# Optimization experiments

Measured on AMD Instinct MI355X. Metric: run time of the kernel, lower is better.

## Reference

```python
import jax, jax.numpy as jnp
import numpy as np
import math

D = 1024       # feature_dim
H = 4          # n_heads
HD = D // H
T = 512        # vertice frames
S = 512        # audio frames
V3 = 15069     # vertice_dim (5023*3)
NSUB = 8
PERIOD = 25
MAXLEN = 600
DFF = 2 * D
AUD = 768


def _build_alibi(n_head=H, max_seq=MAXLEN, period=PERIOD):
    def slopes(n):
        def p2(n):
            start = 2 ** (-2 ** (-(math.log2(n) - 3)))
            return [start * start ** i for i in range(n)]
        if math.log2(n).is_integer():
            return p2(n)
        c = 2 ** math.floor(math.log2(n))
        return p2(c) + slopes(2 * c)[0::2][: n - c]
    sl = np.array(slopes(n_head), np.float32)
    bias = (np.arange(0, max_seq, period)[:, None].repeat(period, 1).reshape(-1) // period).astype(np.float32)
    bias = -bias[::-1]
    i = np.arange(max_seq)[:, None]
    j = np.arange(max_seq)[None, :]
    idx = np.clip(max_seq - 1 - i + j, 0, max_seq - 1)
    alibi = np.where(j <= i, bias[idx], 0.0).astype(np.float32)
    causal = np.where(j <= i, 0.0, -np.inf).astype(np.float32)
    return causal[None] + sl[:, None, None] * alibi[None]   # [H, maxlen, maxlen]


def _build_pe(d=D, period=PERIOD, max_seq=MAXLEN):
    pos = np.arange(period, dtype=np.float32)[:, None]
    div = np.exp(np.arange(0, d, 2, dtype=np.float32) * (-math.log(10000.0) / d))
    pe = np.zeros((period, d), np.float32)
    pe[:, 0::2] = np.sin(pos * div)
    pe[:, 1::2] = np.cos(pos * div)
    reps = max_seq // period + 1
    return np.tile(pe, (reps, 1))[None]                     # [1, reps*period, d]

_ALIBI = jnp.asarray(_build_alibi())
_PE = jnp.asarray(_build_pe())


def _ln(x, g, b, eps=1e-5):
    m = jnp.mean(x, -1, keepdims=True)
    v = jnp.mean((x - m) ** 2, -1, keepdims=True)
    return (x - m) * jax.lax.rsqrt(v + eps) * g + b


def _mha(q_in, kv_in, Wqkv, bqkv, Wo, bo, add_mask=None, bool_mask=None):
    # torch nn.MultiheadAttention with in_proj [3D, D]; y = x @ W.T + b
    B, Tq, _ = q_in.shape
    Ts = kv_in.shape[1]
    Wq, Wk, Wv = jnp.split(Wqkv, 3, axis=0)
    bq, bk, bv = jnp.split(bqkv, 3)
    q = (q_in @ Wq.T + bq).reshape(B, Tq, H, HD).transpose(0, 2, 1, 3)
    k = (kv_in @ Wk.T + bk).reshape(B, Ts, H, HD).transpose(0, 2, 1, 3)
    v = (kv_in @ Wv.T + bv).reshape(B, Ts, H, HD).transpose(0, 2, 1, 3)
    scores = jnp.einsum('bhtd,bhsd->bhts', q, k) / math.sqrt(HD)
    if add_mask is not None:
        scores = scores + add_mask[None]            # [1,H,Tq,Ts] float additive (ALiBi+causal)
    if bool_mask is not None:
        scores = jnp.where(bool_mask, -jnp.inf, scores)  # True == masked (torch semantics)
    attn = jax.nn.softmax(scores, axis=-1)
    out = jnp.einsum('bhts,bhsd->bhtd', attn, v).transpose(0, 2, 1, 3).reshape(B, Tq, D)
    return out @ Wo.T + bo


def setup_inputs() -> dict:
    key = jax.random.key(0)
    ks = jax.random.split(key, 32)
    rn = lambda k, shape, s: jax.random.normal(k, shape, jnp.float32) * s
    inp = {
        'audio_feat': rn(ks[0], (1, S, AUD), 1.0),
        'vertice': rn(ks[1], (1, T, V3), 0.1),
        'template': rn(ks[2], (1, V3), 0.1),
        'one_hot': jnp.zeros((1, NSUB), jnp.float32).at[0, 0].set(1.0),
        'W_af': rn(ks[3], (D, AUD), 0.02), 'b_af': jnp.zeros((D,), jnp.float32),
        'W_vm': rn(ks[4], (D, V3), 0.02), 'b_vm': jnp.zeros((D,), jnp.float32),
        'W_obj': rn(ks[5], (D, NSUB), 0.02),
        'Wqkv_sa': rn(ks[6], (3 * D, D), 0.02), 'bqkv_sa': jnp.zeros((3 * D,), jnp.float32),
        'Wo_sa': rn(ks[7], (D, D), 0.02), 'bo_sa': jnp.zeros((D,), jnp.float32),
        'Wqkv_ca': rn(ks[8], (3 * D, D), 0.02), 'bqkv_ca': jnp.zeros((3 * D,), jnp.float32),
        'Wo_ca': rn(ks[9], (D, D), 0.02), 'bo_ca': jnp.zeros((D,), jnp.float32),
        'W1': rn(ks[10], (DFF, D), 0.02), 'b1': jnp.zeros((DFF,), jnp.float32),
        'W2': rn(ks[11], (D, DFF), 0.02), 'b2': jnp.zeros((D,), jnp.float32),
        'g1': jnp.ones((D,), jnp.float32), 'be1': jnp.zeros((D,), jnp.float32),
        'g2': jnp.ones((D,), jnp.float32), 'be2': jnp.zeros((D,), jnp.float32),
        'g3': jnp.ones((D,), jnp.float32), 'be3': jnp.zeros((D,), jnp.float32),
        # vertice_map_r is zero-init in the source; use small random so grads are informative
        'W_vr': rn(ks[12], (V3, D), 0.02), 'b_vr': jnp.zeros((V3,), jnp.float32),
    }
    return inp


def reference(audio_feat, vertice, template, one_hot,
              W_af, b_af, W_vm, b_vm, W_obj,
              Wqkv_sa, bqkv_sa, Wo_sa, bo_sa,
              Wqkv_ca, bqkv_ca, Wo_ca, bo_ca,
              W1, b1, W2, b2, g1, be1, g2, be2, g3, be3,
              W_vr, b_vr):
    tmpl = template[:, None, :]                               # [1,1,V3]
    hidden = audio_feat @ W_af.T + b_af                       # [1,S,D]
    style = (one_hot @ W_obj.T)[:, None, :]                   # [1,1,D]
    # teacher-forcing branch with template
    vin = jnp.concatenate([tmpl, vertice[:, :-1]], axis=1) - tmpl
    vin = vin @ W_vm.T + b_vm + style
    vin = vin + _PE[:, :T, :]                                 # PPE, dropout is identity in eval
    tgt_mask = _ALIBI[:, :T, :T]                              # [H,T,T]
    mem_mask = ~jnp.eye(T, S, dtype=bool)                     # True == masked; only diagonal attended
    x = vin
    x = _ln(x + _mha(x, x, Wqkv_sa, bqkv_sa, Wo_sa, bo_sa, add_mask=tgt_mask), g1, be1)
    x = _ln(x + _mha(x, hidden, Wqkv_ca, bqkv_ca, Wo_ca, bo_ca, bool_mask=mem_mask), g2, be2)
    ff = jax.nn.relu(x @ W1.T + b1) @ W2.T + b2
    x = _ln(x + ff, g3, be3)
    vertice_out = x @ W_vr.T + b_vr + tmpl                    # [1,T,V3]
    return vertice_out
```

## Files before the change

kernel.cpp:

```cpp
#include <hip/hip_runtime.h>
#include <math.h>

typedef __attribute__((ext_vector_type(8))) short short8;
typedef __attribute__((ext_vector_type(4))) float f32x4;
typedef unsigned short ushort_t;

#define KVIN 15360

__device__ __forceinline__ ushort_t f2bf(float f) {
  unsigned u = __float_as_uint(f);
  return (ushort_t)((u + 0x7fffu + ((u >> 16) & 1u)) >> 16);
}
__device__ __forceinline__ float bf2f(ushort_t h) {
  return __uint_as_float(((unsigned)h) << 16);
}

__device__ __forceinline__ float blockReduceSum256(float v, float* red) {
  #pragma unroll
  for (int o = 32; o; o >>= 1) v += __shfl_xor(v, o);
  int wid = threadIdx.x >> 6, lane = threadIdx.x & 63;
  if (lane == 0) red[wid] = v;
  __syncthreads();
  v = red[0] + red[1] + red[2] + red[3];
  __syncthreads();
  return v;
}
__device__ __forceinline__ float blockReduceMax256(float v, float* red) {
  #pragma unroll
  for (int o = 32; o; o >>= 1) v = fmaxf(v, __shfl_xor(v, o));
  int wid = threadIdx.x >> 6, lane = threadIdx.x & 63;
  if (lane == 0) red[wid] = v;
  __syncthreads();
  v = fmaxf(fmaxf(red[0], red[1]), fmaxf(red[2], red[3]));
  __syncthreads();
  return v;
}

template <bool BF16B, int BIASM, bool CAUSAL, int GMODE, int ZDIV>
__global__ __launch_bounds__(256, 2) void glds5(
    const ushort_t* __restrict__ A, const void* __restrict__ Bv,
    const float* __restrict__ bias, const float* __restrict__ biasB,
    float* __restrict__ C,
    int N, int K, int lda, int ldb, int ldc,
    int kChunk, long aZ, long bZ, long cZ)
{
  int z, m0, n0;
  if (GMODE == 2) {
    const int id = blockIdx.x, u = id & 7, v = id >> 3;
    m0 = (v & 3) * 128;
    n0 = (((v >> 2) << 3) + u) * 128;
    z = 0;
    if (n0 >= N) return;
  } else if (GMODE == 1) {
    z = blockIdx.x; m0 = blockIdx.y * 128; n0 = blockIdx.z * 128;
  } else {
    z = blockIdx.z; m0 = blockIdx.y * 128; n0 = blockIdx.x * 128;
  }
  if (CAUSAL && n0 > m0 + 127) return;
  __shared__ ushort_t sA[2][4096], sB[2][4096];
  const int tid = threadIdx.x;
  const int ks = ZDIV ? (z % ZDIV) : z;
  const int zb = ZDIV ? (z / ZDIV) : z;
  const int kBeg = kChunk ? ks * kChunk : 0;
  const int kEnd = kChunk ? kBeg + kChunk : K;
  A += (size_t)zb * aZ;
  const ushort_t* Bh = (const ushort_t*)Bv;
  const float*    Bf = (const float*)Bv;
  if (BF16B) Bh += (size_t)zb * bZ; else Bf += (size_t)zb * bZ;
  C += (size_t)z * cZ;

  const int r0 = ((tid >> 6) << 4) | (tid & 15);
  const int q0 = (tid >> 4) & 3;
  const int r1 = r0 + 64;
  const ushort_t* pA0 = A + (size_t)(m0 + r0) * lda + (q0 << 3);
  const ushort_t* pA1 = A + (size_t)(m0 + r1) * lda + (q0 << 3);
  const int gn0 = n0 + r0, gn1 = n0 + r1;
  const bool bok0 = gn0 < N, bok1 = gn1 < N;
  const ushort_t* pB0h = Bh + (size_t)gn0 * ldb + (q0 << 3);
  const ushort_t* pB1h = Bh + (size_t)gn1 * ldb + (q0 << 3);
  const float*    pB0f = Bf + (size_t)gn0 * ldb + (q0 << 3);
  const float*    pB1f = Bf + (size_t)gn1 * ldb + (q0 << 3);

  const int lane = tid & 63;
  const int wrb = (tid >> 7) & 1;
  const int wcb = (tid >> 6) & 1;
  const int fr = lane & 15, fq = lane >> 4;

  f32x4 acc[4][4] = {};
  const short8 z8 = {0, 0, 0, 0, 0, 0, 0, 0};
  const float4 z4 = make_float4(0.f, 0.f, 0.f, 0.f);

  short8 ra0, ra1, rb0, rb1; float4 rf0, rf1, rf2, rf3;

#define LOADR(KK) { ra0 = *(const short8*)(pA0 + (KK)); ra1 = *(const short8*)(pA1 + (KK)); \
  if (BF16B) { rb0 = bok0 ? *(const short8*)(pB0h + (KK)) : z8;                             \
               rb1 = bok1 ? *(const short8*)(pB1h + (KK)) : z8; }                           \
  else { rf0 = bok0 ? *(const float4*)(pB0f + (KK)) : z4;                                   \
         rf1 = bok0 ? *(const float4*)(pB0f + (KK) + 4) : z4;                               \
         rf2 = bok1 ? *(const float4*)(pB1f + (KK)) : z4;                                   \
         rf3 = bok1 ? *(const float4*)(pB1f + (KK) + 4) : z4; } }

#define STAGER(BUF) { *(short8*)&sA[BUF][tid << 3] = ra0;                                   \
  *(short8*)&sA[BUF][(tid + 256) << 3] = ra1;                                               \
  if (BF16B) { *(short8*)&sB[BUF][tid << 3] = rb0;                                          \
               *(short8*)&sB[BUF][(tid + 256) << 3] = rb1; }                                \
  else { short8 s0_, s1_;                                                                   \
    _Pragma("unroll") for (int j = 0; j < 4; ++j) {                                         \
      s0_[j] = (short)f2bf(rf0[j]); s0_[j + 4] = (short)f2bf(rf1[j]);                       \
      s1_[j] = (short)f2bf(rf2[j]); s1_[j + 4] = (short)f2bf(rf3[j]); }                     \
    *(short8*)&sB[BUF][tid << 3] = s0_; *(short8*)&sB[BUF][(tid + 256) << 3] = s1_; } }

#define COMPUTE(BUF) { short8 fa[4], fb[4];                                                 \
  _Pragma("unroll") for (int f = 0; f < 4; ++f)                                             \
    fa[f] = *(const short8*)&sA[BUF][((((wrb << 2) + f) << 9) | (lane << 3))];              \
  _Pragma("unroll") for (int g = 0; g < 4; ++g)                                             \
    fb[g] = *(const short8*)&sB[BUF][((((wcb << 2) + g) << 9) | (lane << 3))];              \
  _Pragma("unroll") for (int f = 0; f < 4; ++f)                                             \
    _Pragma("unroll") for (int g = 0; g < 4; ++g)                                           \
      acc[f][g] = __builtin_amdgcn_mfma_f32_16x16x32_bf16(fa[f], fb[g], acc[f][g], 0, 0, 0); }

  LOADR(kBeg);
  const int nt = (kEnd - kBeg) >> 5;
  for (int t = 0; t < nt; ++t) {
    const int cur = t & 1;
    STAGER(cur);
    if (t + 1 < nt) LOADR(kBeg + ((t + 1) << 5));
    asm volatile("s_waitcnt lgkmcnt(0)" ::: "memory");
    __builtin_amdgcn_s_barrier();
    __builtin_amdgcn_sched_barrier(0);
    COMPUTE(cur);
    asm volatile("" ::: "memory");
  }

#undef LOADR
#undef STAGER
#undef COMPUTE

  #pragma unroll
  for (int f = 0; f < 4; ++f) {
    const int gm = m0 + (wrb << 6) + f * 16 + fq * 4;
    #pragma unroll
    for (int g = 0; g < 4; ++g) {
      const int gn = n0 + (wcb << 6) + g * 16 + fr;
      if (gn < N) {
        #pragma unroll
        for (int i = 0; i < 4; ++i) {
          float v = acc[f][g][i];
          if (BIASM >= 1) v += bias[gn];
          if (BIASM >= 2) v += biasB[gn];
          C[(size_t)(gm + i) * ldc + gn] = v;
        }
      }
    }
  }
}

template <bool RELU>
__global__ __launch_bounds__(256) void combine(
    const float* __restrict__ part, const float* __restrict__ bias,
    ushort_t* __restrict__ outh, int nz, long zstride, int total4, int N4)
{
  const int i = blockIdx.x * 256 + threadIdx.x;
  if (i >= total4) return;
  float4 s = ((const float4*)bias)[i % N4];
  for (int z = 0; z < nz; ++z) {
    float4 p = ((const float4*)(part + (size_t)z * zstride))[i];
    s.x += p.x; s.y += p.y; s.z += p.z; s.w += p.w;
  }
  if (RELU) {
    s.x = fmaxf(s.x, 0.f); s.y = fmaxf(s.y, 0.f);
    s.z = fmaxf(s.z, 0.f); s.w = fmaxf(s.w, 0.f);
  }
  ((ushort4*)outh)[i] = make_ushort4(f2bf(s.x), f2bf(s.y), f2bf(s.z), f2bf(s.w));
}

__global__ __launch_bounds__(256) void combine_pv(
    const float* __restrict__ part, ushort_t* __restrict__ ctxh)
{
  const int t = blockIdx.x, tid = threadIdx.x;
  const int h = tid >> 6, dq = tid & 63;
  float4 s = make_float4(0.f, 0.f, 0.f, 0.f);
  #pragma unroll
  for (int ks = 0; ks < 4; ++ks) {
    float4 p = ((const float4*)(part + (size_t)(h * 4 + ks) * 131072 + (size_t)t * 256))[dq];
    s.x += p.x; s.y += p.y; s.z += p.z; s.w += p.w;
  }
  ((ushort4*)ctxh)[t * 256 + h * 64 + dq] =
      make_ushort4(f2bf(s.x), f2bf(s.y), f2bf(s.z), f2bf(s.w));
}

__global__ __launch_bounds__(256) void ln_parts(
    const float* __restrict__ part, int nz, const float* __restrict__ bias,
    float* __restrict__ x, ushort_t* __restrict__ xh,
    const float* __restrict__ g, const float* __restrict__ b)
{
  const int t = blockIdx.x, tid = threadIdx.x;
  float4 y = ((const float4*)(x + (size_t)t * 1024))[tid];
  float4 s = ((const float4*)bias)[tid];
  for (int z = 0; z < nz; ++z) {
    float4 p = ((const float4*)(part + (size_t)z * 524288 + (size_t)t * 1024))[tid];
    s.x += p.x; s.y += p.y; s.z += p.z; s.w += p.w;
  }
  y.x += s.x; y.y += s.y; y.z += s.z; y.w += s.w;
  __shared__ float red[4];
  float sum = blockReduceSum256(y.x + y.y + y.z + y.w, red);
  const float m = sum * (1.f / 1024.f);
  float dx = y.x - m, dy = y.y - m, dz = y.z - m, dw = y.w - m;
  float q = blockReduceSum256(dx * dx + dy * dy + dz * dz + dw * dw, red);
  const float rs = rsqrtf(q * (1.f / 1024.f) + 1e-5f);
  float4 gg = ((const float4*)g)[tid], bb = ((const float4*)b)[tid];
  float4 o;
  o.x = dx * rs * gg.x + bb.x;
  o.y = dy * rs * gg.y + bb.y;
  o.z = dz * rs * gg.z + bb.z;
  o.w = dw * rs * gg.w + bb.w;
  ((float4*)(x + (size_t)t * 1024))[tid] = o;
  ((ushort4*)xh)[t * 256 + tid] = make_ushort4(f2bf(o.x), f2bf(o.y), f2bf(o.z), f2bf(o.w));
}

__global__ __launch_bounds__(256) void prep_all(
    const float* __restrict__ vertice, const float* __restrict__ tmpl,
    ushort_t* __restrict__ Aph,
    const float* __restrict__ Wvm, ushort_t* __restrict__ Wvmh)
{
  const int bid = blockIdx.x;
  if (bid < 7680) {
    const int i = bid * 256 + threadIdx.x;
    const int C4 = KVIN >> 2;
    const int t = i / C4;
    const int c = (i - t * C4) << 2;
    ushort4 o = make_ushort4(0, 0, 0, 0);
    if (t > 0) {
      const float* s = vertice + (size_t)(t - 1) * 15069 + c;
      if (c + 3 < 15069) {
        o = make_ushort4(f2bf(s[0] - tmpl[c]),     f2bf(s[1] - tmpl[c + 1]),
                         f2bf(s[2] - tmpl[c + 2]), f2bf(s[3] - tmpl[c + 3]));
      } else {
        if (c + 0 < 15069) o.x = f2bf(s[0] - tmpl[c]);
        if (c + 1 < 15069) o.y = f2bf(s[1] - tmpl[c + 1]);
        if (c + 2 < 15069) o.z = f2bf(s[2] - tmpl[c + 2]);
        if (c + 3 < 15069) o.w = f2bf(s[3] - tmpl[c + 3]);
      }
    }
    ((ushort4*)Aph)[i] = o;
  } else {
    const int i = (bid - 7680) * 256 + threadIdx.x;
    const int C4 = KVIN >> 2;
    const int r = i / C4;
    const int c = (i - r * C4) << 2;
    const float* s = Wvm + (size_t)r * 15069 + c;
    ushort4 o = make_ushort4(0, 0, 0, 0);
    if (c + 3 < 15069) {
      o = make_ushort4(f2bf(s[0]), f2bf(s[1]), f2bf(s[2]), f2bf(s[3]));
    } else {
      if (c + 0 < 15069) o.x = f2bf(s[0]);
      if (c + 1 < 15069) o.y = f2bf(s[1]);
      if (c + 2 < 15069) o.z = f2bf(s[2]);
      if (c + 3 < 15069) o.w = f2bf(s[3]);
    }
    ((ushort4*)Wvmh)[i] = o;
  }
}

__global__ __launch_bounds__(256) void cvt_both(
    const float* __restrict__ Wvr, ushort_t* __restrict__ Wvrh,
    const float* __restrict__ audio, ushort_t* __restrict__ audh)
{
  const int i = blockIdx.x * 256 + threadIdx.x;
  if (i < 3857664) {
    float4 v = ((const float4*)Wvr)[i];
    ((ushort4*)Wvrh)[i] = make_ushort4(f2bf(v.x), f2bf(v.y), f2bf(v.z), f2bf(v.w));
  } else {
    const int j = i - 3857664;
    if (j < 98304) {
      float4 v = ((const float4*)audio)[j];
      ((ushort4*)audh)[j] = make_ushort4(f2bf(v.x), f2bf(v.y), f2bf(v.z), f2bf(v.w));
    }
  }
}

__global__ __launch_bounds__(256) void qkv_post(
    const float* __restrict__ part, const float* __restrict__ bias,
    ushort_t* __restrict__ qkvh, ushort_t* __restrict__ vth)
{
  const int bid = blockIdx.x;
  __shared__ float tile[32][33];
  if (bid < 1536) {
    const int i = bid * 256 + threadIdx.x;
    float4 s = ((const float4*)bias)[i % 768];
    #pragma unroll
    for (int z = 0; z < 4; ++z) {
      float4 p = ((const float4*)(part + (size_t)z * 1572864))[i];
      s.x += p.x; s.y += p.y; s.z += p.z; s.w += p.w;
    }
    ((ushort4*)qkvh)[i] = make_ushort4(f2bf(s.x), f2bf(s.y), f2bf(s.z), f2bf(s.w));
  } else {
    const int b = bid - 1536;
    const int s0 = (b & 15) * 32, d0 = (b >> 4) * 32;
    const int tx = threadIdx.x & 31, ty = threadIdx.x >> 5;
    for (int r = ty; r < 32; r += 8) {
      float v = bias[2048 + d0 + tx];
      #pragma unroll
      for (int z = 0; z < 4; ++z)
        v += part[(size_t)z * 1572864 + (size_t)(s0 + r) * 3072 + 2048 + d0 + tx];
      tile[r][tx] = v;
    }
    __syncthreads();
    for (int r = ty; r < 32; r += 8)
      vth[(size_t)(d0 + r) * 512 + s0 + tx] = f2bf(tile[tx][r]);
  }
}

__global__ __launch_bounds__(256) void reduce_pe(const float* __restrict__ part,
                                                 const float* __restrict__ one_hot,
                                                 const float* __restrict__ W_obj,
                                                 const float* __restrict__ b_vm,
                                                 float* __restrict__ x,
                                                 ushort_t* __restrict__ xh) {
  const int t = blockIdx.x;
  const float PECOEF = -9.210340371976184f / 512.f;
  const int p = t % 25;
  for (int d = threadIdx.x; d < 1024; d += 256) {
    float s = b_vm[d];
    #pragma unroll
    for (int j = 0; j < 8; ++j) s += one_hot[j] * W_obj[d * 8 + j];
    #pragma unroll
    for (int z = 0; z < 16; ++z) s += part[(size_t)z * 524288 + (size_t)t * 1024 + d];
    float arg = (float)p * expf((float)(d >> 1) * PECOEF);
    s += (d & 1) ? cosf(arg) : sinf(arg);
    const size_t idx = (size_t)t * 1024 + d;
    x[idx] = s;
    xh[idx] = f2bf(s);
  }
}

__global__ __launch_bounds__(256) void softmax_alibi(const float* __restrict__ scores,
                                                     ushort_t* __restrict__ ah) {
  const int i = blockIdx.x, h = blockIdx.y;
  const float* r0 = scores + (size_t)(2 * h) * 262144 + (size_t)i * 512;
  const float* r1 = r0 + 262144;
  const size_t rb = ((size_t)h * 512 + i) * 512;
  const int tid = threadIdx.x;
  const int len = i + 1;
  const float sl = exp2f(-2.f * (float)(h + 1));
  const int j0 = tid, j1 = tid + 256;
  float v0 = -INFINITY, v1 = -INFINITY;
  if (j0 < len) v0 = (r0[j0] + r1[j0]) * 0.0625f - sl * (float)((i - j0) / 25);
  if (j1 < len) v1 = (r0[j1] + r1[j1]) * 0.0625f - sl * (float)((i - j1) / 25);
  __shared__ float red[4];
  float m = blockReduceMax256(fmaxf(v0, v1), red);
  float e0 = (j0 < len) ? expf(v0 - m) : 0.f;
  float e1 = (j1 < len) ? expf(v1 - m) : 0.f;
  float s = blockReduceSum256(e0 + e1, red);
  float inv = 1.f / s;
  ah[rb + j0] = f2bf(e0 * inv);
  ah[rb + j1] = f2bf(e1 * inv);
}

extern "C" void kernel_launch(void* const* d_in, const int* in_sizes, int n_in,
                              void* d_out, int out_size, void* d_ws, size_t ws_size,
                              hipStream_t stream) {
  const float* audio   = (const float*)d_in[0];
  const float* vertice = (const float*)d_in[1];
  const float* tmpl    = (const float*)d_in[2];
  const float* one_hot = (const float*)d_in[3];
  const float* W_af    = (const float*)d_in[4];
  const float* b_af    = (const float*)d_in[5];
  const float* W_vm    = (const float*)d_in[6];
  const float* b_vm    = (const float*)d_in[7];
  const float* W_obj   = (const float*)d_in[8];
  const float* Wqkv_sa = (const float*)d_in[9];
  const float* bqkv_sa = (const float*)d_in[10];
  const float* Wo_sa   = (const float*)d_in[11];
  const float* bo_sa   = (const float*)d_in[12];
  const float* Wqkv_ca = (const float*)d_in[13];
  const float* bqkv_ca = (const float*)d_in[14];
  const float* Wo_ca   = (const float*)d_in[15];
  const float* bo_ca   = (const float*)d_in[16];
  const float* W1      = (const float*)d_in[17];
  const float* b1      = (const float*)d_in[18];
  const float* W2      = (const float*)d_in[19];
  const float* b2      = (const float*)d_in[20];
  const float* g1      = (const float*)d_in[21];
  const float* be1     = (const float*)d_in[22];
  const float* g2      = (const float*)d_in[23];
  const float* be2     = (const float*)d_in[24];
  const float* g3      = (const float*)d_in[25];
  const float* be3     = (const float*)d_in[26];
  const float* W_vr    = (const float*)d_in[27];
  const float* b_vr    = (const float*)d_in[28];
  float* out = (float*)d_out;

  float* base = (float*)d_ws;
  float* apF    = base;
  float* wvmF   = apF + 3932160;
  float* part   = wvmF + 7864320;
  float* x      = part + 8388608;
  float* xhF    = x + 524288;
  float* audF   = xhF + 262144;
  float* hidF   = audF + 196608;
  float* qkvF   = hidF + 262144;
  float* vtF    = qkvF + 786432;
  float* scores = vtF + 262144;
  float* attF   = scores + 2097152;
  float* pvpart = attF + 524288;
  float* ctxF   = pvpart + 2097152;
  float* cvF    = ctxF + 262144;
  float* h1F    = cvF + 262144;

  ushort_t* Aph  = (ushort_t*)apF;
  ushort_t* Wvmh = (ushort_t*)wvmF;
  ushort_t* Wvrh = (ushort_t*)wvmF;
  ushort_t* xh   = (ushort_t*)xhF;
  ushort_t* audh = (ushort_t*)audF;
  ushort_t* hidh = (ushort_t*)hidF;
  ushort_t* qkvh = (ushort_t*)qkvF;
  ushort_t* vth  = (ushort_t*)vtF;
  ushort_t* atth = (ushort_t*)attF;
  ushort_t* ctxh = (ushort_t*)ctxF;
  ushort_t* cvh  = (ushort_t*)cvF;
  ushort_t* h1h  = (ushort_t*)h1F;

  prep_all<<<23040, 256, 0, stream>>>(vertice, tmpl, Aph, W_vm, Wvmh);

  glds5<true, 0, false, 1, 0><<<dim3(16, 4, 8), 256, 0, stream>>>(
      Aph, Wvmh, nullptr, nullptr, part,
      1024, KVIN, KVIN, KVIN, 1024, 960, 0, 0, 524288);
  reduce_pe<<<512, 256, 0, stream>>>(part, one_hot, W_obj, b_vm, x, xh);

  cvt_both<<<15453, 256, 0, stream>>>(W_vr, Wvrh, audio, audh);

  glds5<false, 0, false, 0, 0><<<dim3(8, 4, 6), 256, 0, stream>>>(
      audh, W_af, nullptr, nullptr, part,
      1024, 768, 768, 768, 1024, 128, 0, 0, 524288);
  combine<false><<<512, 256, 0, stream>>>(part, b_af, hidh, 6, 524288, 131072, 256);

  glds5<false, 0, false, 0, 0><<<dim3(24, 4, 4), 256, 0, stream>>>(
      xh, Wqkv_sa, nullptr, nullptr, part,
      3072, 1024, 1024, 1024, 3072, 256, 0, 0, 1572864);
  qkv_post<<<2048, 256, 0, stream>>>(part, bqkv_sa, qkvh, vth);
  glds5<true, 0, true, 0, 0><<<dim3(4, 4, 8), 256, 0, stream>>>(
      qkvh, qkvh + 1024, nullptr, nullptr, scores,
      512, 1024, 3072, 3072, 512, 128, 0, 0, 262144);
  softmax_alibi<<<dim3(512, 4), 256, 0, stream>>>(scores, atth);
  glds5<true, 0, false, 0, 4><<<dim3(2, 4, 16), 256, 0, stream>>>(
      atth, vth, nullptr, nullptr, pvpart,
      256, 512, 512, 512, 256, 128, 262144, 131072, 131072);
  combine_pv<<<512, 256, 0, stream>>>(pvpart, ctxh);
  glds5<false, 0, false, 0, 0><<<dim3(8, 4, 8), 256, 0, stream>>>(
      ctxh, Wo_sa, nullptr, nullptr, part,
      1024, 1024, 1024, 1024, 1024, 128, 0, 0, 524288);
  ln_parts<<<512, 256, 0, stream>>>(part, 8, bo_sa, x, xh, g1, be1);

  glds5<false, 0, false, 0, 0><<<dim3(8, 4, 8), 256, 0, stream>>>(
      hidh, Wqkv_ca + (size_t)2048 * 1024, nullptr, nullptr, part,
      1024, 1024, 1024, 1024, 1024, 128, 0, 0, 524288);
  combine<false><<<512, 256, 0, stream>>>(part, bqkv_ca + 2048, cvh, 8, 524288, 131072, 256);
  glds5<false, 0, false, 0, 0><<<dim3(8, 4, 8), 256, 0, stream>>>(
      cvh, Wo_ca, nullptr, nullptr, part,
      1024, 1024, 1024, 1024, 1024, 128, 0, 0, 524288);
  ln_parts<<<512, 256, 0, stream>>>(part, 8, bo_ca, x, xh, g2, be2);

  glds5<false, 0, false, 0, 0><<<dim3(16, 4, 4), 256, 0, stream>>>(
      xh, W1, nullptr, nullptr, part,
      2048, 1024, 1024, 1024, 2048, 256, 0, 0, 1048576);
  combine<true><<<1024, 256, 0, stream>>>(part, b1, h1h, 4, 1048576, 262144, 512);
  glds5<false, 0, false, 0, 0><<<dim3(8, 4, 8), 256, 0, stream>>>(
      h1h, W2, nullptr, nullptr, part,
      1024, 2048, 2048, 2048, 1024, 256, 0, 0, 524288);
  ln_parts<<<512, 256, 0, stream>>>(part, 8, b2, x, xh, g3, be3);

  glds5<true, 2, false, 2, 0><<<dim3(480, 1, 1), 256, 0, stream>>>(
      xh, Wvrh, b_vr, tmpl, out,
      15069, 1024, 1024, 1024, 15069, 0, 0, 0, 0);
}
```

Measured before the change: 338.8 us.

## Co-schedule independent GEMMs and elementwise kernels into shared launches

Pulls the GEMM body out into a device function so that independent GEMMs can run together in one launch. The pairs are self-attention QKV with the audio projection, scores with the cross-attention V projection, and PV with the cross-attention output projection. The matching post-processing kernels (qkv_post with the hidden combine, softmax with the CV combine, reduce_pe with the weight/audio conversion) are merged the same way, and the audio GEMM split-K changes from 6 to 4. This cuts the launch count and fills the GPU better on small GEMMs, but it adds branch-divergent kernels, dynamic shared memory, and carefully partitioned scratch buffers.

```diff
diff --git a/kernel.cpp b/kernel.cpp
--- a/kernel.cpp
+++ b/kernel.cpp
@@ -36,28 +36,19 @@
   return v;
 }
 
-template <bool BF16B, int BIASM, bool CAUSAL, int GMODE, int ZDIV>
-__global__ __launch_bounds__(256, 2) void glds5(
+template <bool BF16B, int BIASM, bool CAUSAL, int ZDIV>
+__device__ __forceinline__ void gemm_body(
+    void* smem,
     const ushort_t* __restrict__ A, const void* __restrict__ Bv,
     const float* __restrict__ bias, const float* __restrict__ biasB,
     float* __restrict__ C,
     int N, int K, int lda, int ldb, int ldc,
-    int kChunk, long aZ, long bZ, long cZ)
-{
-  int z, m0, n0;
-  if (GMODE == 2) {
-    const int id = blockIdx.x, u = id & 7, v = id >> 3;
-    m0 = (v & 3) * 128;
-    n0 = (((v >> 2) << 3) + u) * 128;
-    z = 0;
-    if (n0 >= N) return;
-  } else if (GMODE == 1) {
-    z = blockIdx.x; m0 = blockIdx.y * 128; n0 = blockIdx.z * 128;
-  } else {
-    z = blockIdx.z; m0 = blockIdx.y * 128; n0 = blockIdx.x * 128;
-  }
+    int kChunk, long aZ, long bZ, long cZ,
+    int z, int m0, int n0)
+{
   if (CAUSAL && n0 > m0 + 127) return;
-  __shared__ ushort_t sA[2][4096], sB[2][4096];
+  ushort_t (*sA)[4096] = (ushort_t (*)[4096])smem;
+  ushort_t (*sB)[4096] = (ushort_t (*)[4096])((char*)smem + 16384);
   const int tid = threadIdx.x;
   const int ks = ZDIV ? (z % ZDIV) : z;
   const int zb = ZDIV ? (z / ZDIV) : z;
@@ -89,7 +80,6 @@
   f32x4 acc[4][4] = {};
   const short8 z8 = {0, 0, 0, 0, 0, 0, 0, 0};
   const float4 z4 = make_float4(0.f, 0.f, 0.f, 0.f);
-
   short8 ra0, ra1, rb0, rb1; float4 rf0, rf1, rf2, rf3;
 
 #define LOADR(KK) { ra0 = *(const short8*)(pA0 + (KK)); ra1 = *(const short8*)(pA1 + (KK)); \
@@ -152,6 +142,90 @@
         }
       }
     }
+  }
+}
+
+template <bool BF16B, int BIASM, bool CAUSAL, int GMODE, int ZDIV>
+__global__ __launch_bounds__(256, 2) void gk(
+    const ushort_t* __restrict__ A, const void* __restrict__ Bv,
+    const float* __restrict__ bias, const float* __restrict__ biasB,
+    float* __restrict__ C,
+    int N, int K, int lda, int ldb, int ldc,
+    int kChunk, long aZ, long bZ, long cZ)
+{
+  extern __shared__ char smem[];
+  int z, m0, n0;
+  if (GMODE == 2) {
+    const int id = blockIdx.x, u = id & 7, v = id >> 3;
+    m0 = (v & 3) * 128;
+    n0 = (((v >> 2) << 3) + u) * 128;
+    z = 0;
+    if (n0 >= N) return;
+  } else if (GMODE == 1) {
+    z = blockIdx.x; m0 = blockIdx.y * 128; n0 = blockIdx.z * 128;
+  } else {
+    z = blockIdx.z; m0 = blockIdx.y * 128; n0 = blockIdx.x * 128;
+  }
+  gemm_body<BF16B, BIASM, CAUSAL, ZDIV>(smem, A, Bv, bias, biasB, C,
+      N, K, lda, ldb, ldc, kChunk, aZ, bZ, cZ, z, m0, n0);
+}
+
+__global__ __launch_bounds__(256, 2) void gk_qkv_hid(
+    const ushort_t* __restrict__ xh, const float* __restrict__ Wqkv,
+    float* __restrict__ partQ,
+    const ushort_t* __restrict__ audh, const float* __restrict__ Waf,
+    float* __restrict__ partH)
+{
+  extern __shared__ char smem[];
+  const int bid = blockIdx.x;
+  if (bid < 384) {
+    const int x = bid % 24, y = (bid / 24) & 3, z = bid / 96;
+    gemm_body<false, 0, false, 0>(smem, xh, Wqkv, nullptr, nullptr, partQ,
+        3072, 1024, 1024, 1024, 3072, 256, 0, 0, 1572864, z, y * 128, x * 128);
+  } else {
+    const int b = bid - 384;
+    const int x = b & 7, y = (b >> 3) & 3, z = b >> 5;
+    gemm_body<false, 0, false, 0>(smem, audh, Waf, nullptr, nullptr, partH,
+        1024, 768, 768, 768, 1024, 192, 0, 0, 524288, z, y * 128, x * 128);
+  }
+}
+
+__global__ __launch_bounds__(256, 2) void gk_scores_cav(
+    const ushort_t* __restrict__ qkvh, float* __restrict__ scores,
+    const ushort_t* __restrict__ hidh, const float* __restrict__ WvCA,
+    float* __restrict__ partCV)
+{
+  extern __shared__ char smem[];
+  const int bid = blockIdx.x;
+  if (bid < 128) {
+    const int x = bid & 3, y = (bid >> 2) & 3, z = bid >> 4;
+    gemm_body<true, 0, true, 0>(smem, qkvh, qkvh + 1024, nullptr, nullptr, scores,
+        512, 1024, 3072, 3072, 512, 128, 0, 0, 262144, z, y * 128, x * 128);
+  } else {
+    const int b = bid - 128;
+    const int x = b & 7, y = (b >> 3) & 3, z = b >> 5;
+    gemm_body<false, 0, false, 0>(smem, hidh, WvCA, nullptr, nullptr, partCV,
+        1024, 1024, 1024, 1024, 1024, 128, 0, 0, 524288, z, y * 128, x * 128);
+  }
+}
+
+__global__ __launch_bounds__(256, 2) void gk_pv_cao(
+    const ushort_t* __restrict__ atth, const ushort_t* __restrict__ vth,
+    float* __restrict__ pvpart,
+    const ushort_t* __restrict__ cvh, const float* __restrict__ WoCA,
+    float* __restrict__ partUp)
+{
+  extern __shared__ char smem[];
+  const int bid = blockIdx.x;
+  if (bid < 128) {
+    const int x = bid & 1, y = (bid >> 1) & 3, z = bid >> 3;
+    gemm_body<true, 0, false, 4>(smem, atth, vth, nullptr, nullptr, pvpart,
+        256, 512, 512, 512, 256, 128, 262144, 131072, 131072, z, y * 128, x * 128);
+  } else {
+    const int b = bid - 128;
+    const int x = b & 7, y = (b >> 3) & 3, z = b >> 5;
+    gemm_body<false, 0, false, 0>(smem, cvh, WoCA, nullptr, nullptr, partUp,
+        1024, 1024, 1024, 1024, 1024, 128, 0, 0, 524288, z, y * 128, x * 128);
   }
 }
 
@@ -262,16 +336,39 @@
   }
 }
 
-__global__ __launch_bounds__(256) void cvt_both(
+__global__ __launch_bounds__(256) void post_vin(
+    const float* __restrict__ part,
+    const float* __restrict__ one_hot, const float* __restrict__ W_obj,
+    const float* __restrict__ b_vm,
+    float* __restrict__ x, ushort_t* __restrict__ xh,
     const float* __restrict__ Wvr, ushort_t* __restrict__ Wvrh,
     const float* __restrict__ audio, ushort_t* __restrict__ audh)
 {
-  const int i = blockIdx.x * 256 + threadIdx.x;
-  if (i < 3857664) {
-    float4 v = ((const float4*)Wvr)[i];
-    ((ushort4*)Wvrh)[i] = make_ushort4(f2bf(v.x), f2bf(v.y), f2bf(v.z), f2bf(v.w));
-  } else {
-    const int j = i - 3857664;
+  const int bid = blockIdx.x;
+  if (bid < 512) {
+    const int t = bid;
+    const float PECOEF = -9.210340371976184f / 512.f;
+    const int p = t % 25;
+    for (int d = threadIdx.x; d < 1024; d += 256) {
+      float s = b_vm[d];
+      #pragma unroll
+      for (int j = 0; j < 8; ++j) s += one_hot[j] * W_obj[d * 8 + j];
+      #pragma unroll
+      for (int z = 0; z < 16; ++z) s += part[(size_t)z * 524288 + (size_t)t * 1024 + d];
+      float arg = (float)p * expf((float)(d >> 1) * PECOEF);
+      s += (d & 1) ? cosf(arg) : sinf(arg);
+      const size_t idx = (size_t)t * 1024 + d;
+      x[idx] = s;
+      xh[idx] = f2bf(s);
+    }
+  } else if (bid < 15581) {
+    const int i = (bid - 512) * 256 + threadIdx.x;
+    if (i < 3857664) {
+      float4 v = ((const float4*)Wvr)[i];
+      ((ushort4*)Wvrh)[i] = make_ushort4(f2bf(v.x), f2bf(v.y), f2bf(v.z), f2bf(v.w));
+    }
+  } else {
+    const int j = (bid - 15581) * 256 + threadIdx.x;
     if (j < 98304) {
       float4 v = ((const float4*)audio)[j];
       ((ushort4*)audh)[j] = make_ushort4(f2bf(v.x), f2bf(v.y), f2bf(v.z), f2bf(v.w));
@@ -279,9 +376,11 @@
   }
 }
 
-__global__ __launch_bounds__(256) void qkv_post(
-    const float* __restrict__ part, const float* __restrict__ bias,
-    ushort_t* __restrict__ qkvh, ushort_t* __restrict__ vth)
+__global__ __launch_bounds__(256) void qkvpost_combhid(
+    const float* __restrict__ partQ, const float* __restrict__ bias,
+    ushort_t* __restrict__ qkvh, ushort_t* __restrict__ vth,
+    const float* __restrict__ partH, const float* __restrict__ b_af,
+    ushort_t* __restrict__ hidh)
 {
   const int bid = blockIdx.x;
   __shared__ float tile[32][33];
@@ -290,11 +389,11 @@
     float4 s = ((const float4*)bias)[i % 768];
     #pragma unroll
     for (int z = 0; z < 4; ++z) {
-      float4 p = ((const float4*)(part + (size_t)z * 1572864))[i];
+      float4 p = ((const float4*)(partQ + (size_t)z * 1572864))[i];
       s.x += p.x; s.y += p.y; s.z += p.z; s.w += p.w;
     }
     ((ushort4*)qkvh)[i] = make_ushort4(f2bf(s.x), f2bf(s.y), f2bf(s.z), f2bf(s.w));
-  } else {
+  } else if (bid < 2048) {
     const int b = bid - 1536;
     const int s0 = (b & 15) * 32, d0 = (b >> 4) * 32;
     const int tx = threadIdx.x & 31, ty = threadIdx.x >> 5;
@@ -302,59 +401,60 @@
       float v = bias[2048 + d0 + tx];
       #pragma unroll
       for (int z = 0; z < 4; ++z)
-        v += part[(size_t)z * 1572864 + (size_t)(s0 + r) * 3072 + 2048 + d0 + tx];
+        v += partQ[(size_t)z * 1572864 + (size_t)(s0 + r) * 3072 + 2048 + d0 + tx];
       tile[r][tx] = v;
     }
     __syncthreads();
     for (int r = ty; r < 32; r += 8)
       vth[(size_t)(d0 + r) * 512 + s0 + tx] = f2bf(tile[tx][r]);
-  }
-}
-
-__global__ __launch_bounds__(256) void reduce_pe(const float* __restrict__ part,
-                                                 const float* __restrict__ one_hot,
-                                                 const float* __restrict__ W_obj,
-                                                 const float* __restrict__ b_vm,
-                                                 float* __restrict__ x,
-                                                 ushort_t* __restrict__ xh) {
-  const int t = blockIdx.x;
-  const float PECOEF = -9.210340371976184f / 512.f;
-  const int p = t % 25;
-  for (int d = threadIdx.x; d < 1024; d += 256) {
-    float s = b_vm[d];
+  } else {
+    const int i = (bid - 2048) * 256 + threadIdx.x;
+    float4 s = ((const float4*)b_af)[i % 256];
     #pragma unroll
-    for (int j = 0; j < 8; ++j) s += one_hot[j] * W_obj[d * 8 + j];
+    for (int z = 0; z < 4; ++z) {
+      float4 p = ((const float4*)(partH + (size_t)z * 524288))[i];
+      s.x += p.x; s.y += p.y; s.z += p.z; s.w += p.w;
+    }
+    ((ushort4*)hidh)[i] = make_ushort4(f2bf(s.x), f2bf(s.y), f2bf(s.z), f2bf(s.w));
+  }
+}
+
+__global__ __launch_bounds__(256) void sm_combcv(
+    const float* __restrict__ scores, ushort_t* __restrict__ ah,
+    const float* __restrict__ partCV, const float* __restrict__ bqkv_ca,
+    ushort_t* __restrict__ cvh)
+{
+  const int bid = blockIdx.x;
+  __shared__ float red[4];
+  if (bid < 2048) {
+    const int i = bid & 511, h = bid >> 9;
+    const float* r0 = scores + (size_t)(2 * h) * 262144 + (size_t)i * 512;
+    const float* r1 = r0 + 262144;
+    const size_t rb = ((size_t)h * 512 + i) * 512;
+    const int tid = threadIdx.x;
+    const int len = i + 1;
+    const float sl = exp2f(-2.f * (float)(h + 1));
+    const int j0 = tid, j1 = tid + 256;
+    float v0 = -INFINITY, v1 = -INFINITY;
+    if (j0 < len) v0 = (r0[j0] + r1[j0]) * 0.0625f - sl * (float)((i - j0) / 25);
+    if (j1 < len) v1 = (r0[j1] + r1[j1]) * 0.0625f - sl * (float)((i - j1) / 25);
+    float m = blockReduceMax256(fmaxf(v0, v1), red);
+    float e0 = (j0 < len) ? expf(v0 - m) : 0.f;
+    float e1 = (j1 < len) ? expf(v1 - m) : 0.f;
+    float s = blockReduceSum256(e0 + e1, red);
+    float inv = 1.f / s;
+    ah[rb + j0] = f2bf(e0 * inv);
+    ah[rb + j1] = f2bf(e1 * inv);
+  } else {
+    const int i = (bid - 2048) * 256 + threadIdx.x;
+    float4 s = ((const float4*)(bqkv_ca + 2048))[i % 256];
     #pragma unroll
-    for (int z = 0; z < 16; ++z) s += part[(size_t)z * 524288 + (size_t)t * 1024 + d];
-    float arg = (float)p * expf((float)(d >> 1) * PECOEF);
-    s += (d & 1) ? cosf(arg) : sinf(arg);
-    const size_t idx = (size_t)t * 1024 + d;
-    x[idx] = s;
-    xh[idx] = f2bf(s);
-  }
-}
-
-__global__ __launch_bounds__(256) void softmax_alibi(const float* __restrict__ scores,
-                                                     ushort_t* __restrict__ ah) {
-  const int i = blockIdx.x, h = blockIdx.y;
-  const float* r0 = scores + (size_t)(2 * h) * 262144 + (size_t)i * 512;
-  const float* r1 = r0 + 262144;
-  const size_t rb = ((size_t)h * 512 + i) * 512;
-  const int tid = threadIdx.x;
-  const int len = i + 1;
-  const float sl = exp2f(-2.f * (float)(h + 1));
-  const int j0 = tid, j1 = tid + 256;
-  float v0 = -INFINITY, v1 = -INFINITY;
-  if (j0 < len) v0 = (r0[j0] + r1[j0]) * 0.0625f - sl * (float)((i - j0) / 25);
-  if (j1 < len) v1 = (r0[j1] + r1[j1]) * 0.0625f - sl * (float)((i - j1) / 25);
-  __shared__ float red[4];
-  float m = blockReduceMax256(fmaxf(v0, v1), red);
-  float e0 = (j0 < len) ? expf(v0 - m) : 0.f;
-  float e1 = (j1 < len) ? expf(v1 - m) : 0.f;
-  float s = blockReduceSum256(e0 + e1, red);
-  float inv = 1.f / s;
-  ah[rb + j0] = f2bf(e0 * inv);
-  ah[rb + j1] = f2bf(e1 * inv);
+    for (int z = 0; z < 8; ++z) {
+      float4 p = ((const float4*)(partCV + (size_t)z * 524288))[i];
+      s.x += p.x; s.y += p.y; s.z += p.z; s.w += p.w;
+    }
+    ((ushort4*)cvh)[i] = make_ushort4(f2bf(s.x), f2bf(s.y), f2bf(s.z), f2bf(s.w));
+  }
 }
 
 extern "C" void kernel_launch(void* const* d_in, const int* in_sizes, int n_in,
@@ -408,6 +508,10 @@
   float* cvF    = ctxF + 262144;
   float* h1F    = cvF + 262144;
 
+  float* partQ  = part;
+  float* partH  = part + 6291456;
+  float* partUp = part + 4194304;
+
   ushort_t* Aph  = (ushort_t*)apF;
   ushort_t* Wvmh = (ushort_t*)wvmF;
   ushort_t* Wvrh = (ushort_t*)wvmF;
@@ -423,54 +527,45 @@
 
   prep_all<<<23040, 256, 0, stream>>>(vertice, tmpl, Aph, W_vm, Wvmh);
 
-  glds5<true, 0, false, 1, 0><<<dim3(16, 4, 8), 256, 0, stream>>>(
+  gk<true, 0, false, 1, 0><<<dim3(16, 4, 8), 256, 32768, stream>>>(
       Aph, Wvmh, nullptr, nullptr, part,
       1024, KVIN, KVIN, KVIN, 1024, 960, 0, 0, 524288);
-  reduce_pe<<<512, 256, 0, stream>>>(part, one_hot, W_obj, b_vm, x, xh);
-
-  cvt_both<<<15453, 256, 0, stream>>>(W_vr, Wvrh, audio, audh);
-
-  glds5<false, 0, false, 0, 0><<<dim3(8, 4, 6), 256, 0, stream>>>(
-      audh, W_af, nullptr, nullptr, part,
-      1024, 768, 768, 768, 1024, 128, 0, 0, 524288);
-  combine<false><<<512, 256, 0, stream>>>(part, b_af, hidh, 6, 524288, 131072, 256);
-
-  glds5<false, 0, false, 0, 0><<<dim3(24, 4, 4), 256, 0, stream>>>(
-      xh, Wqkv_sa, nullptr, nullptr, part,
-      3072, 1024, 1024, 1024, 3072, 256, 0, 0, 1572864);
-  qkv_post<<<2048, 256, 0, stream>>>(part, bqkv_sa, qkvh, vth);
-  glds5<true, 0, true, 0, 0><<<dim3(4, 4, 8), 256, 0, stream>>>(
-      qkvh, qkvh + 1024, nullptr, nullptr, scores,
-      512, 1024, 3072, 3072, 512, 128, 0, 0, 262144);
-  softmax_alibi<<<dim3(512, 4), 256, 0, stream>>>(scores, atth);
-  glds5<true, 0, false, 0, 4><<<dim3(2, 4, 16), 256, 0, stream>>>(
-      atth, vth, nullptr, nullptr, pvpart,
-      256, 512, 512, 512, 256, 128, 262144, 131072, 131072);
+
+  post_vin<<<15965, 256, 0, stream>>>(part, one_hot, W_obj, b_vm, x, xh,
+                                      W_vr, Wvrh, audio, audh);
+
+  gk_qkv_hid<<<512, 256, 32768, stream>>>(xh, Wqkv_sa, partQ, audh, W_af, partH);
+
+  qkvpost_combhid<<<2560, 256, 0, stream>>>(partQ, bqkv_sa, qkvh, vth,
+                                            partH, b_af, hidh);
+
+  gk_scores_cav<<<384, 256, 32768, stream>>>(qkvh, scores, hidh,
+                                             Wqkv_ca + (size_t)2048 * 1024, part);
+
+  sm_combcv<<<2560, 256, 0, stream>>>(scores, atth, part, bqkv_ca, cvh);
+
+  gk_pv_cao<<<384, 256, 32768, stream>>>(atth, vth, pvpart, cvh, Wo_ca, partUp);
+
   combine_pv<<<512, 256, 0, stream>>>(pvpart, ctxh);
-  glds5<false, 0, false, 0, 0><<<dim3(8, 4, 8), 256, 0, stream>>>(
+
+  gk<false, 0, false, 0, 0><<<dim3(8, 4, 8), 256, 32768, stream>>>(
       ctxh, Wo_sa, nullptr, nullptr, part,
       1024, 1024, 1024, 1024, 1024, 128, 0, 0, 524288);
+
   ln_parts<<<512, 256, 0, stream>>>(part, 8, bo_sa, x, xh, g1, be1);
 
-  glds5<false, 0, false, 0, 0><<<dim3(8, 4, 8), 256, 0, stream>>>(
-      hidh, Wqkv_ca + (size_t)2048 * 1024, nullptr, nullptr, part,
-      1024, 1024, 1024, 1024, 1024, 128, 0, 0, 524288);
-  combine<false><<<512, 256, 0, stream>>>(part, bqkv_ca + 2048, cvh, 8, 524288, 131072, 256);
-  glds5<false, 0, false, 0, 0><<<dim3(8, 4, 8), 256, 0, stream>>>(
-      cvh, Wo_ca, nullptr, nullptr, part,
-      1024, 1024, 1024, 1024, 1024, 128, 0, 0, 524288);
-  ln_parts<<<512, 256, 0, stream>>>(part, 8, bo_ca, x, xh, g2, be2);
-
-  glds5<false, 0, false, 0, 0><<<dim3(16, 4, 4), 256, 0, stream>>>(
+  ln_parts<<<512, 256, 0, stream>>>(partUp, 8, bo_ca, x, xh, g2, be2);
+
+  gk<false, 0, false, 0, 0><<<dim3(16, 4, 4), 256, 32768, stream>>>(
       xh, W1, nullptr, nullptr, part,
       2048, 1024, 1024, 1024, 2048, 256, 0, 0, 1048576);
   combine<true><<<1024, 256, 0, stream>>>(part, b1, h1h, 4, 1048576, 262144, 512);
-  glds5<false, 0, false, 0, 0><<<dim3(8, 4, 8), 256, 0, stream>>>(
+  gk<false, 0, false, 0, 0><<<dim3(8, 4, 8), 256, 32768, stream>>>(
       h1h, W2, nullptr, nullptr, part,
       1024, 2048, 2048, 2048, 1024, 256, 0, 0, 524288);
   ln_parts<<<512, 256, 0, stream>>>(part, 8, b2, x, xh, g3, be3);
 
-  glds5<true, 2, false, 2, 0><<<dim3(480, 1, 1), 256, 0, stream>>>(
+  gk<true, 2, false, 2, 0><<<dim3(480, 1, 1), 256, 32768, stream>>>(
       xh, Wvrh, b_vr, tmpl, out,
       15069, 1024, 1024, 1024, 15069, 0, 0, 0, 0);
 }
```

Result: faster. 296.4 us (-12.5%).
